# Kernel optimization log

Hardware: AMD Instinct MI355X
Metric: run time of the kernel (lower is better)

The kernel has to match this reference:

```python
import jax, jax.numpy as jnp
import numpy as np

ATOL = 1e-3   # torch.isclose atol used in the original
RTOL = 1e-5   # torch.isclose default rtol
B, H, W = 8, 2048, 2048


def _sample_one(x, key):
    """Rejection-sample uniform noise until mean((x > prob)) ~ mean(x).
    Faithful to the per-sample while-loop in ThresholdSigmoidMaskFunction.forward."""
    target = jnp.mean(x)

    def draw(k):
        k, sub = jax.random.split(k)
        return k, jax.random.uniform(sub, x.shape, dtype=x.dtype)

    def cond(state):
        _, prob = state
        m = jnp.mean((x > prob).astype(x.dtype))
        # torch.isclose: |a - b| <= atol + rtol*|b| ; loop while NOT close
        return jnp.abs(m - target) > (ATOL + RTOL * jnp.abs(target))

    def body(state):
        k, _ = state
        return draw(k)

    key, prob0 = draw(key)
    _, prob = jax.lax.while_loop(cond, body, (key, prob0))
    result = (x > prob).astype(x.dtype)
    return result, prob


def setup_inputs() -> dict:
    key = jax.random.key(0)
    # probabilities in [0,1] -- required for the rejection loop to terminate
    input_probs = jax.random.uniform(key, (B, H, W), dtype=jnp.float32)
    return {"input_probs": input_probs}


def reference(input_probs):
    batch = input_probs.shape[0]
    keys = jax.random.split(jax.random.key(42), batch)
    results, _probs = jax.vmap(_sample_one)(input_probs, keys)
    return results
```

## Files before the change

### kernel.cpp

```cpp
#include <hip/hip_runtime.h>
#include <stdint.h>
#include <math.h>

#define BATCH 8
#define NPB   4194304u
#define BPB   256
#define EPB   16384u

#if defined(__has_builtin)
#if __has_builtin(__builtin_amdgcn_ballot_w64)
#define HAS_BALLOT64 1
#endif
#endif

typedef float f32x4 __attribute__((ext_vector_type(4)));

struct Ws {
  double   psum[BATCH][BPB];
  uint32_t pcnt[BATCH][BPB];
};

struct Keys {
  uint32_t a0[BATCH], a1[BATCH];
  uint32_t b0[BATCH], b1[BATCH];
};

__host__ __device__ __forceinline__ uint32_t rotl_h(uint32_t x, int n) {
  return (x << n) | (x >> (32 - n));
}

#ifdef __HIP_DEVICE_COMPILE__
#define ROTL(x, n) __builtin_amdgcn_alignbit((x), (x), 32 - (n))
#else
#define ROTL(x, n) rotl_h((x), (n))
#endif

__host__ __device__ __forceinline__ void tf2x32(uint32_t k0, uint32_t k1,
                                                uint32_t x0, uint32_t x1,
                                                uint32_t& y0, uint32_t& y1) {
  uint32_t k2 = k0 ^ k1 ^ 0x1BD11BDAu;
  x0 += k0; x1 += k1;
#define R4A x0+=x1; x1=ROTL(x1,13); x1^=x0; x0+=x1; x1=ROTL(x1,15); x1^=x0; \
            x0+=x1; x1=ROTL(x1,26); x1^=x0; x0+=x1; x1=ROTL(x1, 6); x1^=x0;
#define R4B x0+=x1; x1=ROTL(x1,17); x1^=x0; x0+=x1; x1=ROTL(x1,29); x1^=x0; \
            x0+=x1; x1=ROTL(x1,16); x1^=x0; x0+=x1; x1=ROTL(x1,24); x1^=x0;
  R4A x0 += k1; x1 += k2 + 1u;
  R4B x0 += k2; x1 += k0 + 2u;
  R4A x0 += k0; x1 += k1 + 3u;
  R4B x0 += k1; x1 += k2 + 4u;
  R4A x0 += k2; x1 += k0 + 5u;
#undef R4A
#undef R4B
  y0 = x0; y1 = x1;
}

__device__ __forceinline__ uint32_t tf_bits(uint32_t s0, uint32_t s1, uint32_t j) {
  uint32_t y0, y1;
  tf2x32(s0, s1, 0u, j, y0, y1);
  return y0 ^ y1;
}

__device__ __forceinline__ float u01(uint32_t b) {
#ifdef __HIP_DEVICE_COMPILE__
  return __uint_as_float(__builtin_amdgcn_alignbit(0x7Fu, b, 9)) - 1.0f;
#else
  return __uint_as_float((b >> 9) | 0x3f800000u) - 1.0f;
#endif
}

__global__ __launch_bounds__(256) void k_main(const float* __restrict__ x,
                                              float* __restrict__ out,
                                              Ws* __restrict__ ws, Keys keys) {
  const int b = blockIdx.y;
  const uint32_t s0 = keys.a0[b], s1 = keys.a1[b];
  const uint32_t base = blockIdx.x * EPB + threadIdx.x * 4u;
  const float* __restrict__ pA = x + (size_t)b * NPB + base;
  float*       __restrict__ qA = out + (size_t)b * NPB + base;

  uint32_t c = 0;
  float    sf = 0.0f;
  uint32_t j = base;

#pragma unroll 1
  for (int it = 0; it < 8; ++it) {
    f32x4 xa = __builtin_nontemporal_load((const f32x4*)(pA));
    f32x4 xc = __builtin_nontemporal_load((const f32x4*)(pA + 1024));
    f32x4 oa, oc;
#ifdef HAS_BALLOT64
#define CNT(p) c += (uint32_t)__builtin_popcountll(__builtin_amdgcn_ballot_w64(p))
#else
#define CNT(p) c += (uint32_t)(p)
#endif
#define DOPAIR(k, off) {                                                  \
      bool p0 = xa[k] > u01(tf_bits(s0, s1, j + off));                    \
      bool p1 = xc[k] > u01(tf_bits(s0, s1, j + off + 1024u));            \
      oa[k] = p0 ? 1.0f : 0.0f; oc[k] = p1 ? 1.0f : 0.0f;                 \
      CNT(p0); CNT(p1); }
    DOPAIR(0, 0u) DOPAIR(1, 1u) DOPAIR(2, 2u) DOPAIR(3, 3u)
#undef DOPAIR
#undef CNT
    sf += ((xa[0] + xa[1]) + (xa[2] + xa[3])) + ((xc[0] + xc[1]) + (xc[2] + xc[3]));
    __builtin_nontemporal_store(oa, (f32x4*)(qA));
    __builtin_nontemporal_store(oc, (f32x4*)(qA + 1024));
    pA += 2048; qA += 2048; j += 2048u;
  }

  double S = (double)sf;
  for (int off = 32; off > 0; off >>= 1) S += __shfl_down(S, off, 64);
#ifndef HAS_BALLOT64
  for (int off = 32; off > 0; off >>= 1) c += __shfl_down(c, off, 64);
#endif

  __shared__ double   sS[4];
  __shared__ uint32_t sC[4];
  const int lane = threadIdx.x & 63, wave = threadIdx.x >> 6;
  if (lane == 0) { sS[wave] = S; sC[wave] = c; }
  __syncthreads();
  if (threadIdx.x == 0) {
    ws->psum[b][blockIdx.x] = (sS[0] + sS[1]) + (sS[2] + sS[3]);
    ws->pcnt[b][blockIdx.x] = (sC[0] + sC[1]) + (sC[2] + sC[3]);
  }
}

__global__ __launch_bounds__(256) void k_resolve(const float* __restrict__ x,
                                                 float* __restrict__ out,
                                                 Ws* __restrict__ ws, Keys keys) {
  const int b = blockIdx.y;

  double   S = ws->psum[b][threadIdx.x];
  uint32_t c = ws->pcnt[b][threadIdx.x];
  for (int off = 32; off > 0; off >>= 1) {
    c += __shfl_down(c, off, 64);
    S += __shfl_down(S, off, 64);
  }
  __shared__ double   sS[4];
  __shared__ uint32_t sC[4];
  __shared__ int      sAccept;
  const int lane = threadIdx.x & 63, wave = threadIdx.x >> 6;
  if (lane == 0) { sS[wave] = S; sC[wave] = c; }
  __syncthreads();
  if (threadIdx.x == 0) {
    double St = (sS[0] + sS[1]) + (sS[2] + sS[3]);
    uint32_t Ct = (sC[0] + sC[1]) + (sC[2] + sC[3]);
    float target = (float)(St / (double)NPB);
    float thr    = 1e-3f + 1e-5f * fabsf(target);
    float m      = (float)Ct * (1.0f / (float)NPB);
    sAccept = (fabsf(m - target) <= thr) ? 1 : 0;
  }
  __syncthreads();
  if (sAccept) return;

  const uint32_t s0 = keys.b0[b], s1 = keys.b1[b];
  const uint32_t blkbase = blockIdx.x * EPB;
  const float* xb = x + (size_t)b * NPB;
  float*       ob = out + (size_t)b * NPB;
#pragma unroll 1
  for (int it = 0; it < 8; ++it) {
    const uint32_t j = blkbase + (uint32_t)it * 2048u + threadIdx.x * 4u;
    float4 xa = *(const float4*)(xb + j);
    float4 xc = *(const float4*)(xb + j + 1024u);
    float4 oa, oc;
#define FPAIR(comp, off) {                                                \
      oa.comp = (xa.comp > u01(tf_bits(s0, s1, j + off))) ? 1.0f : 0.0f;  \
      oc.comp = (xc.comp > u01(tf_bits(s0, s1, j + off + 1024u))) ? 1.0f : 0.0f; }
    FPAIR(x, 0u) FPAIR(y, 1u) FPAIR(z, 2u) FPAIR(w, 3u)
#undef FPAIR
    *(float4*)(ob + j)         = oa;
    *(float4*)(ob + j + 1024u) = oc;
  }
}

extern "C" void kernel_launch(void* const* d_in, const int* in_sizes, int n_in,
                              void* d_out, int out_size, void* d_ws, size_t ws_size,
                              hipStream_t stream) {
  const float* x = (const float*)d_in[0];
  float* out = (float*)d_out;
  Ws* ws = (Ws*)d_ws;

  Keys keys;
  for (int b = 0; b < BATCH; ++b) {
    uint32_t k0, k1, n0, n1, s0, s1;
    tf2x32(0u, 42u, 0u, (uint32_t)b, k0, k1);
    tf2x32(k0, k1, 0u, 1u, s0, s1);
    keys.a0[b] = s0; keys.a1[b] = s1;
    tf2x32(k0, k1, 0u, 0u, n0, n1);
    tf2x32(n0, n1, 0u, 1u, s0, s1);
    keys.b0[b] = s0; keys.b1[b] = s1;
  }

  hipLaunchKernelGGL(k_main,    dim3(BPB, BATCH), dim3(256), 0, stream, x, out, ws, keys);
  hipLaunchKernelGGL(k_resolve, dim3(BPB, BATCH), dim3(256), 0, stream, x, out, ws, keys);
}
```

Measured before the change: 258.7 us.

## Fuse main and resolve kernels via atomic last-block reduction and prefetch loads

Replaces the two-kernel scheme with a single kernel. Each block atomically adds its partial sum and count to per-batch totals, and the last block to arrive decides acceptance. If a batch is rejected, that one block redraws the whole batch alone. The change also software-prefetches the next iteration's loads, fully unrolls the loop, drops the nontemporal load/store hints, and adds a memset of the workspace. This removes the second kernel launch and its 2048-block grid, at the cost of atomics and a very slow serial fallback whenever a redraw is needed.

```diff
diff --git a/kernel.cpp b/kernel.cpp
--- a/kernel.cpp
+++ b/kernel.cpp
@@ -13,11 +13,10 @@
 #endif
 #endif
 
-typedef float f32x4 __attribute__((ext_vector_type(4)));
-
 struct Ws {
-  double   psum[BATCH][BPB];
-  uint32_t pcnt[BATCH][BPB];
+  double   Ssum[BATCH];
+  uint32_t Csum[BATCH];
+  uint32_t arrive[BATCH];
 };
 
 struct Keys {
@@ -68,9 +67,9 @@
 #endif
 }
 
-__global__ __launch_bounds__(256) void k_main(const float* __restrict__ x,
-                                              float* __restrict__ out,
-                                              Ws* __restrict__ ws, Keys keys) {
+__global__ __launch_bounds__(256) void k_fused(const float* __restrict__ x,
+                                               float* __restrict__ out,
+                                               Ws* __restrict__ ws, Keys keys) {
   const int b = blockIdx.y;
   const uint32_t s0 = keys.a0[b], s1 = keys.a1[b];
   const uint32_t base = blockIdx.x * EPB + threadIdx.x * 4u;
@@ -79,30 +78,37 @@
 
   uint32_t c = 0;
   float    sf = 0.0f;
+
+  float4 xa = *(const float4*)(pA);
+  float4 xc = *(const float4*)(pA + 1024);
   uint32_t j = base;
 
-#pragma unroll 1
+#pragma unroll
   for (int it = 0; it < 8; ++it) {
-    f32x4 xa = __builtin_nontemporal_load((const f32x4*)(pA));
-    f32x4 xc = __builtin_nontemporal_load((const f32x4*)(pA + 1024));
-    f32x4 oa, oc;
+    float4 na = xa, nc = xc;
+    if (it < 7) {
+      na = *(const float4*)(pA + 2048);
+      nc = *(const float4*)(pA + 3072);
+    }
+    float4 oa, oc;
 #ifdef HAS_BALLOT64
 #define CNT(p) c += (uint32_t)__builtin_popcountll(__builtin_amdgcn_ballot_w64(p))
 #else
 #define CNT(p) c += (uint32_t)(p)
 #endif
-#define DOPAIR(k, off) {                                                  \
-      bool p0 = xa[k] > u01(tf_bits(s0, s1, j + off));                    \
-      bool p1 = xc[k] > u01(tf_bits(s0, s1, j + off + 1024u));            \
-      oa[k] = p0 ? 1.0f : 0.0f; oc[k] = p1 ? 1.0f : 0.0f;                 \
+#define DOPAIR(comp, off) {                                               \
+      bool p0 = xa.comp > u01(tf_bits(s0, s1, j + off));                  \
+      bool p1 = xc.comp > u01(tf_bits(s0, s1, j + off + 1024u));          \
+      oa.comp = p0 ? 1.0f : 0.0f; oc.comp = p1 ? 1.0f : 0.0f;             \
       CNT(p0); CNT(p1); }
-    DOPAIR(0, 0u) DOPAIR(1, 1u) DOPAIR(2, 2u) DOPAIR(3, 3u)
+    DOPAIR(x, 0u) DOPAIR(y, 1u) DOPAIR(z, 2u) DOPAIR(w, 3u)
 #undef DOPAIR
 #undef CNT
-    sf += ((xa[0] + xa[1]) + (xa[2] + xa[3])) + ((xc[0] + xc[1]) + (xc[2] + xc[3]));
-    __builtin_nontemporal_store(oa, (f32x4*)(qA));
-    __builtin_nontemporal_store(oc, (f32x4*)(qA + 1024));
+    sf += ((xa.x + xa.y) + (xa.z + xa.w)) + ((xc.x + xc.y) + (xc.z + xc.w));
+    *(float4*)(qA)        = oa;
+    *(float4*)(qA + 1024) = oc;
     pA += 2048; qA += 2048; j += 2048u;
+    xa = na; xc = nc;
   }
 
   double S = (double)sf;
@@ -113,60 +119,48 @@
 
   __shared__ double   sS[4];
   __shared__ uint32_t sC[4];
+  __shared__ int      sLast, sAcc;
   const int lane = threadIdx.x & 63, wave = threadIdx.x >> 6;
   if (lane == 0) { sS[wave] = S; sC[wave] = c; }
   __syncthreads();
   if (threadIdx.x == 0) {
-    ws->psum[b][blockIdx.x] = (sS[0] + sS[1]) + (sS[2] + sS[3]);
-    ws->pcnt[b][blockIdx.x] = (sC[0] + sC[1]) + (sC[2] + sC[3]);
+    double   Sb = (sS[0] + sS[1]) + (sS[2] + sS[3]);
+    uint32_t Cb = (sC[0] + sC[1]) + (sC[2] + sC[3]);
+    atomicAdd(&ws->Ssum[b], Sb);
+    atomicAdd(&ws->Csum[b], Cb);
+    __threadfence();
+    uint32_t old = atomicAdd(&ws->arrive[b], 1u);
+    sLast = (old == BPB - 1u) ? 1 : 0;
   }
-}
+  __syncthreads();
+  if (!sLast) return;
 
-__global__ __launch_bounds__(256) void k_resolve(const float* __restrict__ x,
-                                                 float* __restrict__ out,
-                                                 Ws* __restrict__ ws, Keys keys) {
-  const int b = blockIdx.y;
-
-  double   S = ws->psum[b][threadIdx.x];
-  uint32_t c = ws->pcnt[b][threadIdx.x];
-  for (int off = 32; off > 0; off >>= 1) {
-    c += __shfl_down(c, off, 64);
-    S += __shfl_down(S, off, 64);
-  }
-  __shared__ double   sS[4];
-  __shared__ uint32_t sC[4];
-  __shared__ int      sAccept;
-  const int lane = threadIdx.x & 63, wave = threadIdx.x >> 6;
-  if (lane == 0) { sS[wave] = S; sC[wave] = c; }
-  __syncthreads();
   if (threadIdx.x == 0) {
-    double St = (sS[0] + sS[1]) + (sS[2] + sS[3]);
-    uint32_t Ct = (sC[0] + sC[1]) + (sC[2] + sC[3]);
+    __threadfence();
+    double   St = ws->Ssum[b];
+    uint32_t Ct = ws->Csum[b];
     float target = (float)(St / (double)NPB);
     float thr    = 1e-3f + 1e-5f * fabsf(target);
     float m      = (float)Ct * (1.0f / (float)NPB);
-    sAccept = (fabsf(m - target) <= thr) ? 1 : 0;
+    sAcc = (fabsf(m - target) <= thr) ? 1 : 0;
   }
   __syncthreads();
-  if (sAccept) return;
+  if (sAcc) return;
 
-  const uint32_t s0 = keys.b0[b], s1 = keys.b1[b];
-  const uint32_t blkbase = blockIdx.x * EPB;
-  const float* xb = x + (size_t)b * NPB;
-  float*       ob = out + (size_t)b * NPB;
+  {
+    const uint32_t t0 = keys.b0[b], t1 = keys.b1[b];
+    const float* __restrict__ xb = x + (size_t)b * NPB;
+    float*       __restrict__ ob = out + (size_t)b * NPB;
 #pragma unroll 1
-  for (int it = 0; it < 8; ++it) {
-    const uint32_t j = blkbase + (uint32_t)it * 2048u + threadIdx.x * 4u;
-    float4 xa = *(const float4*)(xb + j);
-    float4 xc = *(const float4*)(xb + j + 1024u);
-    float4 oa, oc;
-#define FPAIR(comp, off) {                                                \
-      oa.comp = (xa.comp > u01(tf_bits(s0, s1, j + off))) ? 1.0f : 0.0f;  \
-      oc.comp = (xc.comp > u01(tf_bits(s0, s1, j + off + 1024u))) ? 1.0f : 0.0f; }
-    FPAIR(x, 0u) FPAIR(y, 1u) FPAIR(z, 2u) FPAIR(w, 3u)
-#undef FPAIR
-    *(float4*)(ob + j)         = oa;
-    *(float4*)(ob + j + 1024u) = oc;
+    for (uint32_t jj = threadIdx.x * 4u; jj < NPB; jj += 1024u) {
+      float4 v = *(const float4*)(xb + jj);
+      float4 o;
+      o.x = (v.x > u01(tf_bits(t0, t1, jj + 0u))) ? 1.0f : 0.0f;
+      o.y = (v.y > u01(tf_bits(t0, t1, jj + 1u))) ? 1.0f : 0.0f;
+      o.z = (v.z > u01(tf_bits(t0, t1, jj + 2u))) ? 1.0f : 0.0f;
+      o.w = (v.w > u01(tf_bits(t0, t1, jj + 3u))) ? 1.0f : 0.0f;
+      *(float4*)(ob + jj) = o;
+    }
   }
 }
 
@@ -188,6 +182,6 @@
     keys.b0[b] = s0; keys.b1[b] = s1;
   }
 
-  hipLaunchKernelGGL(k_main,    dim3(BPB, BATCH), dim3(256), 0, stream, x, out, ws, keys);
-  hipLaunchKernelGGL(k_resolve, dim3(BPB, BATCH), dim3(256), 0, stream, x, out, ws, keys);
+  hipMemsetAsync(d_ws, 0, sizeof(Ws), stream);
+  hipLaunchKernelGGL(k_fused, dim3(BPB, BATCH), dim3(256), 0, stream, x, out, ws, keys);
 }
```

Measured after the change: 352.1 us. +36.1%, slower.
